# Kernel tuning notes

Measured on AMD Instinct MI355X. Metric: run time of the kernel, lower is better.

## Reference

```python
import jax, jax.numpy as jnp
import numpy as np

N_NODES = 101001  # n_user + n_item + n_attr + 1
EMBED = 64
N_EDGES = 2020020  # ~avg degree 20
EPS = 1e-12


def setup_inputs() -> dict:
    key = jax.random.key(0)
    ks = jax.random.split(key, 8)
    h0 = jax.random.normal(ks[0], (N_NODES, EMBED), dtype=jnp.float32)
    h_att = jax.random.normal(ks[1], (N_NODES, EMBED), dtype=jnp.float32)
    t_att = jax.random.normal(ks[2], (N_NODES, EMBED), dtype=jnp.float32)
    w1 = jax.random.normal(ks[3], (EMBED, EMBED), dtype=jnp.float32) * (1.0 / np.sqrt(EMBED))
    b1 = jnp.zeros((EMBED,), dtype=jnp.float32)
    w2 = jax.random.normal(ks[4], (EMBED, EMBED), dtype=jnp.float32) * (1.0 / np.sqrt(EMBED))
    b2 = jnp.zeros((EMBED,), dtype=jnp.float32)
    edge_row = jnp.sort(jax.random.randint(ks[5], (N_EDGES,), 0, N_NODES, dtype=jnp.int32))
    edge_col = jax.random.randint(ks[6], (N_EDGES,), 0, N_NODES, dtype=jnp.int32)
    return {"h0": h0, "h_att": h_att, "t_att": t_att, "w1": w1, "b1": b1,
            "w2": w2, "b2": b2, "edge_row": edge_row, "edge_col": edge_col}


def _edge_softmax(h_att, t_att, edge_row, edge_col, n):
    # per-source-node softmax over ragged neighbor lists (kg_pair)
    logits = jnp.sum(h_att[edge_row] * t_att[edge_col], axis=-1)  # [E]
    m = jax.ops.segment_max(logits, edge_row, num_segments=n)
    e = jnp.exp(logits - m[edge_row])
    s = jax.ops.segment_sum(e, edge_row, num_segments=n)
    return e / jnp.maximum(s[edge_row], EPS)  # [E]


def reference(h0, h_att, t_att, w1, b1, w2, b2, edge_row, edge_col):
    n, d = h0.shape
    w = _edge_softmax(h_att, t_att, edge_row, edge_col, n)  # sparse attention weights
    h = h0
    all_embedding = [h0]
    for (W, b) in ((w1, b1), (w2, b2)):  # k = 1, 2 of ProP_n_Layer
        # n_embedding = SpMM(sp_weight, h)
        msg = jax.ops.segment_sum(w[:, None] * h[edge_col], edge_row, num_segments=n)
        add = h + msg
        h = jax.nn.relu(add @ W.T + b)
        norm = h / jnp.maximum(jnp.linalg.norm(h, axis=-1, keepdims=True), EPS)
        all_embedding.append(norm)
        h = norm  # normalized embedding feeds the next propagation layer
    return jnp.stack(all_embedding, axis=0)  # [n_layer, N, D]
```

## Files before the change

### kernel.cpp

```cpp
#include <hip/hip_runtime.h>
#include <math.h>

#define EMBED 64

__device__ __forceinline__ float dot4(float4 a, float4 b) {
    return fmaf(a.x, b.x, fmaf(a.y, b.y, fmaf(a.z, b.z, a.w * b.w)));
}

__device__ __forceinline__ float red16(float d) {
    d += __shfl_xor(d, 1);
    d += __shfl_xor(d, 2);
    d += __shfl_xor(d, 4);
    d += __shfl_xor(d, 8);
    return d;
}

__global__ void copy_h0_kernel(const float* __restrict__ h0, float* __restrict__ out, int n4) {
    int i = blockIdx.x * blockDim.x + threadIdx.x;
    if (i < n4) ((float4*)out)[i] = ((const float4*)h0)[i];
}

__global__ void build_rowptr_kernel(const int* __restrict__ row, int* __restrict__ rp, int E, int N) {
    int i = blockIdx.x * blockDim.x + threadIdx.x;
    if (i >= E) return;
    if (i == 0) {
        int r0 = row[0];
        for (int r = 0; r <= r0; ++r) rp[r] = 0;
    } else {
        int a = row[i - 1], b = row[i];
        for (int r = a + 1; r <= b; ++r) rp[r] = i;
    }
    if (i == E - 1) {
        int rl = row[E - 1];
        for (int r = rl + 1; r <= N; ++r) rp[r] = E;
    }
}

__global__ void __launch_bounds__(256, 8) edge_logits_kernel(
        const float* __restrict__ ha, const float* __restrict__ ta,
        const int* __restrict__ row, const int* __restrict__ col,
        float* __restrict__ logits, int E, int totalWaves) {
    int wid = (blockIdx.x * blockDim.x + threadIdx.x) >> 6;
    int lane = threadIdx.x & 63;
    int eg = lane >> 4, q = lane & 15;
    const float4* ha4 = (const float4*)ha;
    const float4* ta4 = (const float4*)ta;

    for (int base = wid * 16; base < E; base += totalWaves * 16) {
        int j0 = base + eg, j1 = base + 4 + eg, j2 = base + 8 + eg, j3 = base + 12 + eg;
        int i0 = min(j0, E - 1), i1 = min(j1, E - 1);
        int i2 = min(j2, E - 1), i3 = min(j3, E - 1);
        int r0 = row[i0], r1 = row[i1], r2 = row[i2], r3 = row[i3];
        int c0 = col[i0], c1 = col[i1], c2 = col[i2], c3 = col[i3];
        float4 t0 = ta4[(size_t)c0 * 16 + q];
        float4 t1 = ta4[(size_t)c1 * 16 + q];
        float4 t2 = ta4[(size_t)c2 * 16 + q];
        float4 t3 = ta4[(size_t)c3 * 16 + q];
        float4 a0 = ha4[(size_t)r0 * 16 + q];
        float4 a1 = ha4[(size_t)r1 * 16 + q];
        float4 a2 = ha4[(size_t)r2 * 16 + q];
        float4 a3 = ha4[(size_t)r3 * 16 + q];
        float d0 = red16(dot4(a0, t0));
        float d1 = red16(dot4(a1, t1));
        float d2 = red16(dot4(a2, t2));
        float d3 = red16(dot4(a3, t3));
        if (q == 0) {
            if (j0 < E) logits[j0] = d0;
            if (j1 < E) logits[j1] = d1;
            if (j2 < E) logits[j2] = d2;
            if (j3 < E) logits[j3] = d3;
        }
    }
}

__global__ void __launch_bounds__(256) node_softmax_kernel(
        const int* __restrict__ rp, float* __restrict__ lw, int N) {
    int n = (blockIdx.x * blockDim.x + threadIdx.x) >> 6;
    int lane = threadIdx.x & 63;
    if (n >= N) return;
    int s = rp[n], t = rp[n + 1];
    int deg = t - s;
    if (deg <= 0) return;

    if (deg <= 64) {
        float v = (lane < deg) ? lw[s + lane] : -1e30f;
        float m = v;
        #pragma unroll
        for (int off = 32; off > 0; off >>= 1) m = fmaxf(m, __shfl_xor(m, off));
        float e = (lane < deg) ? __expf(v - m) : 0.f;
        float sum = e;
        #pragma unroll
        for (int off = 32; off > 0; off >>= 1) sum += __shfl_xor(sum, off);
        float inv = 1.f / fmaxf(sum, 1e-12f);
        if (lane < deg) lw[s + lane] = e * inv;
    } else {
        float m = -1e30f;
        for (int e = s + lane; e < t; e += 64) m = fmaxf(m, lw[e]);
        #pragma unroll
        for (int off = 32; off > 0; off >>= 1) m = fmaxf(m, __shfl_xor(m, off));
        float sum = 0.f;
        for (int e = s + lane; e < t; e += 64) sum += __expf(lw[e] - m);
        #pragma unroll
        for (int off = 32; off > 0; off >>= 1) sum += __shfl_xor(sum, off);
        float inv = 1.f / fmaxf(sum, 1e-12f);
        for (int e = s + lane; e < t; e += 64) lw[e] = __expf(lw[e] - m) * inv;
    }
}

__global__ void __launch_bounds__(256, 8) spmm_kernel(
        const float* __restrict__ h_in, const int* __restrict__ col,
        const float* __restrict__ ew, const int* __restrict__ rp,
        float* __restrict__ add_out, int N, int totalWaves) {
    int wid = (blockIdx.x * blockDim.x + threadIdx.x) >> 6;
    int lane = threadIdx.x & 63;
    int eg = lane >> 4, q = lane & 15;
    const float4* h4 = (const float4*)h_in;

    for (int n = wid; n < N; n += totalWaves) {
        int s = rp[n], t = rp[n + 1];
        float4 self = h4[(size_t)n * 16 + q];
        float4 a0 = make_float4(0.f, 0.f, 0.f, 0.f);
        float4 a1 = make_float4(0.f, 0.f, 0.f, 0.f);
        int e0 = s;
        for (; e0 + 16 <= t; e0 += 16) {
            int i0 = e0 + eg, i1 = e0 + 4 + eg, i2 = e0 + 8 + eg, i3 = e0 + 12 + eg;
            int c0 = col[i0], c1 = col[i1], c2 = col[i2], c3 = col[i3];
            float w0 = ew[i0], w1 = ew[i1], w2 = ew[i2], w3 = ew[i3];
            float4 v0 = h4[(size_t)c0 * 16 + q];
            float4 v1 = h4[(size_t)c1 * 16 + q];
            float4 v2 = h4[(size_t)c2 * 16 + q];
            float4 v3 = h4[(size_t)c3 * 16 + q];
            a0.x = fmaf(w0, v0.x, a0.x); a0.y = fmaf(w0, v0.y, a0.y);
            a0.z = fmaf(w0, v0.z, a0.z); a0.w = fmaf(w0, v0.w, a0.w);
            a1.x = fmaf(w1, v1.x, a1.x); a1.y = fmaf(w1, v1.y, a1.y);
            a1.z = fmaf(w1, v1.z, a1.z); a1.w = fmaf(w1, v1.w, a1.w);
            a0.x = fmaf(w2, v2.x, a0.x); a0.y = fmaf(w2, v2.y, a0.y);
            a0.z = fmaf(w2, v2.z, a0.z); a0.w = fmaf(w2, v2.w, a0.w);
            a1.x = fmaf(w3, v3.x, a1.x); a1.y = fmaf(w3, v3.y, a1.y);
            a1.z = fmaf(w3, v3.z, a1.z); a1.w = fmaf(w3, v3.w, a1.w);
        }
        if (e0 < t) {
            int j0 = e0 + eg, j1 = e0 + 4 + eg, j2 = e0 + 8 + eg, j3 = e0 + 12 + eg;
            int i0 = min(j0, t - 1), i1 = min(j1, t - 1);
            int i2 = min(j2, t - 1), i3 = min(j3, t - 1);
            int c0 = col[i0], c1 = col[i1], c2 = col[i2], c3 = col[i3];
            float w0 = (j0 < t) ? ew[i0] : 0.f;
            float w1 = (j1 < t) ? ew[i1] : 0.f;
            float w2 = (j2 < t) ? ew[i2] : 0.f;
            float w3 = (j3 < t) ? ew[i3] : 0.f;
            float4 v0 = h4[(size_t)c0 * 16 + q];
            float4 v1 = h4[(size_t)c1 * 16 + q];
            float4 v2 = h4[(size_t)c2 * 16 + q];
            float4 v3 = h4[(size_t)c3 * 16 + q];
            a0.x = fmaf(w0, v0.x, a0.x); a0.y = fmaf(w0, v0.y, a0.y);
            a0.z = fmaf(w0, v0.z, a0.z); a0.w = fmaf(w0, v0.w, a0.w);
            a1.x = fmaf(w1, v1.x, a1.x); a1.y = fmaf(w1, v1.y, a1.y);
            a1.z = fmaf(w1, v1.z, a1.z); a1.w = fmaf(w1, v1.w, a1.w);
            a0.x = fmaf(w2, v2.x, a0.x); a0.y = fmaf(w2, v2.y, a0.y);
            a0.z = fmaf(w2, v2.z, a0.z); a0.w = fmaf(w2, v2.w, a0.w);
            a1.x = fmaf(w3, v3.x, a1.x); a1.y = fmaf(w3, v3.y, a1.y);
            a1.z = fmaf(w3, v3.z, a1.z); a1.w = fmaf(w3, v3.w, a1.w);
        }
        a0.x += a1.x; a0.y += a1.y; a0.z += a1.z; a0.w += a1.w;
        a0.x += __shfl_xor(a0.x, 16); a0.y += __shfl_xor(a0.y, 16);
        a0.z += __shfl_xor(a0.z, 16); a0.w += __shfl_xor(a0.w, 16);
        a0.x += __shfl_xor(a0.x, 32); a0.y += __shfl_xor(a0.y, 32);
        a0.z += __shfl_xor(a0.z, 32); a0.w += __shfl_xor(a0.w, 32);
        if (eg == 0) {
            float4 r;
            r.x = self.x + a0.x; r.y = self.y + a0.y;
            r.z = self.z + a0.z; r.w = self.w + a0.w;
            ((float4*)add_out)[(size_t)n * 16 + q] = r;
        }
    }
}

__global__ void __launch_bounds__(256, 4) dense_kernel(
        const float* __restrict__ W, const float* __restrict__ b,
        float* __restrict__ io, int N, int totalWaves) {
    __shared__ float4 rbuf[4][17];
    int wid = (blockIdx.x * blockDim.x + threadIdx.x) >> 6;
    int lane = threadIdx.x & 63;
    int ws = threadIdx.x >> 6;

    float4 Wr[16];
    const float4* W4 = (const float4*)W;
    #pragma unroll
    for (int p = 0; p < 16; ++p) Wr[p] = W4[lane * 16 + p];
    float bias = b[lane];
    float* rb = (float*)&rbuf[ws][0];

    float vcur = 0.f;
    if (wid < N) vcur = io[(size_t)wid * EMBED + lane];

    for (int n = wid; n < N; n += totalWaves) {
        rb[lane] = vcur;
        int n2 = n + totalWaves;
        float vnext = 0.f;
        if (n2 < N) vnext = io[(size_t)n2 * EMBED + lane];

        float x0 = bias, x1 = 0.f, x2 = 0.f, x3 = 0.f;
        #pragma unroll
        for (int j = 0; j < 4; ++j) {
            float4 a0 = rbuf[ws][4 * j + 0];
            float4 a1 = rbuf[ws][4 * j + 1];
            float4 a2 = rbuf[ws][4 * j + 2];
            float4 a3 = rbuf[ws][4 * j + 3];
            float4 w0 = Wr[4 * j + 0], w1 = Wr[4 * j + 1];
            float4 w2 = Wr[4 * j + 2], w3 = Wr[4 * j + 3];
            x0 = fmaf(a0.x, w0.x, x0); x0 = fmaf(a0.y, w0.y, x0);
            x0 = fmaf(a0.z, w0.z, x0); x0 = fmaf(a0.w, w0.w, x0);
            x1 = fmaf(a1.x, w1.x, x1); x1 = fmaf(a1.y, w1.y, x1);
            x1 = fmaf(a1.z, w1.z, x1); x1 = fmaf(a1.w, w1.w, x1);
            x2 = fmaf(a2.x, w2.x, x2); x2 = fmaf(a2.y, w2.y, x2);
            x2 = fmaf(a2.z, w2.z, x2); x2 = fmaf(a2.w, w2.w, x2);
            x3 = fmaf(a3.x, w3.x, x3); x3 = fmaf(a3.y, w3.y, x3);
            x3 = fmaf(a3.z, w3.z, x3); x3 = fmaf(a3.w, w3.w, x3);
        }
        float x = fmaxf((x0 + x1) + (x2 + x3), 0.f);

        float ss = x * x;
        #pragma unroll
        for (int off = 32; off > 0; off >>= 1) ss += __shfl_xor(ss, off);
        float scale = 1.f / fmaxf(sqrtf(ss), 1e-12f);
        io[(size_t)n * EMBED + lane] = x * scale;
        vcur = vnext;
    }
}

extern "C" void kernel_launch(void* const* d_in, const int* in_sizes, int n_in,
                              void* d_out, int out_size, void* d_ws, size_t ws_size,
                              hipStream_t stream) {
    const float* h0   = (const float*)d_in[0];
    const float* ha   = (const float*)d_in[1];
    const float* ta   = (const float*)d_in[2];
    const float* w1   = (const float*)d_in[3];
    const float* b1   = (const float*)d_in[4];
    const float* w2   = (const float*)d_in[5];
    const float* b2   = (const float*)d_in[6];
    const int*   erow = (const int*)d_in[7];
    const int*   ecol = (const int*)d_in[8];

    const int N = in_sizes[0] / EMBED;
    const int E = in_sizes[7];
    float* out = (float*)d_out;

    int*   rp = (int*)d_ws;
    size_t rp_bytes = ((size_t)(N + 1) * sizeof(int) + 255) & ~(size_t)255;
    float* ew = (float*)((char*)d_ws + rp_bytes);

    {
        int n4 = N * EMBED / 4;
        copy_h0_kernel<<<(n4 + 255) / 256, 256, 0, stream>>>(h0, out, n4);
    }
    build_rowptr_kernel<<<(E + 255) / 256, 256, 0, stream>>>(erow, rp, E, N);
    edge_logits_kernel<<<2048, 256, 0, stream>>>(ha, ta, erow, ecol, ew, E, 2048 * 4);
    {
        int waves_per_block = 256 / 64;
        int blocks = (N + waves_per_block - 1) / waves_per_block;
        node_softmax_kernel<<<blocks, 256, 0, stream>>>(rp, ew, N);
    }

    float* out1 = out + (size_t)N * EMBED;
    float* out2 = out + 2 * (size_t)N * EMBED;
    spmm_kernel<<<2048, 256, 0, stream>>>(h0, ecol, ew, rp, out1, N, 2048 * 4);
    dense_kernel<<<1024, 256, 0, stream>>>(w1, b1, out1, N, 1024 * 4);
    spmm_kernel<<<2048, 256, 0, stream>>>(out1, ecol, ew, rp, out2, N, 2048 * 4);
    dense_kernel<<<1024, 256, 0, stream>>>(w2, b2, out2, N, 1024 * 4);
}
```

Baseline: 462.1 us.

## Fuse SpMM with dense layer and merge setup kernels to cut launches

Merges the rowptr build into the edge-logits kernel and the h0 copy into the softmax kernel. Fuses each SpMM with its following dense+ReLU+L2-normalize step, passing the aggregated row to the matmul through per-wave LDS instead of a global round trip. This removes four kernel launches and one write plus re-read of the intermediate per layer. In exchange the fused kernel holds the 64-float weight rows in registers, which may lower occupancy for the gather-heavy SpMM part, and it relies on an explicit lgkmcnt wait rather than a barrier for the intra-wave LDS handoff.

Result: faster. 416.7 us, median of 2 (-9.8%).

```diff
diff --git a/kernel.cpp b/kernel.cpp
--- a/kernel.cpp
+++ b/kernel.cpp
@@ -15,32 +15,28 @@
     return d;
 }
 
-__global__ void copy_h0_kernel(const float* __restrict__ h0, float* __restrict__ out, int n4) {
-    int i = blockIdx.x * blockDim.x + threadIdx.x;
-    if (i < n4) ((float4*)out)[i] = ((const float4*)h0)[i];
-}
-
-__global__ void build_rowptr_kernel(const int* __restrict__ row, int* __restrict__ rp, int E, int N) {
-    int i = blockIdx.x * blockDim.x + threadIdx.x;
-    if (i >= E) return;
-    if (i == 0) {
-        int r0 = row[0];
-        for (int r = 0; r <= r0; ++r) rp[r] = 0;
-    } else {
-        int a = row[i - 1], b = row[i];
-        for (int r = a + 1; r <= b; ++r) rp[r] = i;
-    }
-    if (i == E - 1) {
-        int rl = row[E - 1];
-        for (int r = rl + 1; r <= N; ++r) rp[r] = E;
-    }
-}
-
-__global__ void __launch_bounds__(256, 8) edge_logits_kernel(
+__global__ void __launch_bounds__(256, 8) rowptr_logits_kernel(
         const float* __restrict__ ha, const float* __restrict__ ta,
         const int* __restrict__ row, const int* __restrict__ col,
-        float* __restrict__ logits, int E, int totalWaves) {
-    int wid = (blockIdx.x * blockDim.x + threadIdx.x) >> 6;
+        int* __restrict__ rp, float* __restrict__ logits,
+        int E, int N, int totalThreads, int totalWaves) {
+    int tid = blockIdx.x * blockDim.x + threadIdx.x;
+
+    for (int i = tid; i < E; i += totalThreads) {
+        if (i == 0) {
+            int r0 = row[0];
+            for (int r = 0; r <= r0; ++r) rp[r] = 0;
+        } else {
+            int a = row[i - 1], b = row[i];
+            for (int r = a + 1; r <= b; ++r) rp[r] = i;
+        }
+        if (i == E - 1) {
+            int rl = row[E - 1];
+            for (int r = rl + 1; r <= N; ++r) rp[r] = E;
+        }
+    }
+
+    int wid = tid >> 6;
     int lane = threadIdx.x & 63;
     int eg = lane >> 4, q = lane & 15;
     const float4* ha4 = (const float4*)ha;
@@ -73,48 +69,64 @@
     }
 }
 
-__global__ void __launch_bounds__(256) node_softmax_kernel(
-        const int* __restrict__ rp, float* __restrict__ lw, int N) {
-    int n = (blockIdx.x * blockDim.x + threadIdx.x) >> 6;
+__global__ void __launch_bounds__(256) copy_softmax_kernel(
+        const float* __restrict__ h0, float* __restrict__ out0, int n4,
+        const int* __restrict__ rp, float* __restrict__ lw, int N,
+        int totalThreads, int totalWaves) {
+    int tid = blockIdx.x * blockDim.x + threadIdx.x;
+    for (int i = tid; i < n4; i += totalThreads)
+        ((float4*)out0)[i] = ((const float4*)h0)[i];
+
+    int wid = tid >> 6;
     int lane = threadIdx.x & 63;
-    if (n >= N) return;
-    int s = rp[n], t = rp[n + 1];
-    int deg = t - s;
-    if (deg <= 0) return;
-
-    if (deg <= 64) {
-        float v = (lane < deg) ? lw[s + lane] : -1e30f;
-        float m = v;
-        #pragma unroll
-        for (int off = 32; off > 0; off >>= 1) m = fmaxf(m, __shfl_xor(m, off));
-        float e = (lane < deg) ? __expf(v - m) : 0.f;
-        float sum = e;
-        #pragma unroll
-        for (int off = 32; off > 0; off >>= 1) sum += __shfl_xor(sum, off);
-        float inv = 1.f / fmaxf(sum, 1e-12f);
-        if (lane < deg) lw[s + lane] = e * inv;
-    } else {
-        float m = -1e30f;
-        for (int e = s + lane; e < t; e += 64) m = fmaxf(m, lw[e]);
-        #pragma unroll
-        for (int off = 32; off > 0; off >>= 1) m = fmaxf(m, __shfl_xor(m, off));
-        float sum = 0.f;
-        for (int e = s + lane; e < t; e += 64) sum += __expf(lw[e] - m);
-        #pragma unroll
-        for (int off = 32; off > 0; off >>= 1) sum += __shfl_xor(sum, off);
-        float inv = 1.f / fmaxf(sum, 1e-12f);
-        for (int e = s + lane; e < t; e += 64) lw[e] = __expf(lw[e] - m) * inv;
-    }
-}
-
-__global__ void __launch_bounds__(256, 8) spmm_kernel(
-        const float* __restrict__ h_in, const int* __restrict__ col,
-        const float* __restrict__ ew, const int* __restrict__ rp,
-        float* __restrict__ add_out, int N, int totalWaves) {
+    for (int n = wid; n < N; n += totalWaves) {
+        int s = rp[n], t = rp[n + 1];
+        int deg = t - s;
+        if (deg <= 0) continue;
+        if (deg <= 64) {
+            float v = (lane < deg) ? lw[s + lane] : -1e30f;
+            float m = v;
+            #pragma unroll
+            for (int off = 32; off > 0; off >>= 1) m = fmaxf(m, __shfl_xor(m, off));
+            float e = (lane < deg) ? __expf(v - m) : 0.f;
+            float sum = e;
+            #pragma unroll
+            for (int off = 32; off > 0; off >>= 1) sum += __shfl_xor(sum, off);
+            float inv = 1.f / fmaxf(sum, 1e-12f);
+            if (lane < deg) lw[s + lane] = e * inv;
+        } else {
+            float m = -1e30f;
+            for (int e = s + lane; e < t; e += 64) m = fmaxf(m, lw[e]);
+            #pragma unroll
+            for (int off = 32; off > 0; off >>= 1) m = fmaxf(m, __shfl_xor(m, off));
+            float sum = 0.f;
+            for (int e = s + lane; e < t; e += 64) sum += __expf(lw[e] - m);
+            #pragma unroll
+            for (int off = 32; off > 0; off >>= 1) sum += __shfl_xor(sum, off);
+            float inv = 1.f / fmaxf(sum, 1e-12f);
+            for (int e = s + lane; e < t; e += 64) lw[e] = __expf(lw[e] - m) * inv;
+        }
+    }
+}
+
+__global__ void __launch_bounds__(256, 4) prop_layer_kernel(
+        const float* __restrict__ h_in,
+        const float* __restrict__ W, const float* __restrict__ b,
+        const int* __restrict__ col, const float* __restrict__ ew,
+        const int* __restrict__ rp,
+        float* __restrict__ out, int N, int totalWaves) {
+    __shared__ float4 rbuf[4][17];
     int wid = (blockIdx.x * blockDim.x + threadIdx.x) >> 6;
     int lane = threadIdx.x & 63;
+    int ws = threadIdx.x >> 6;
     int eg = lane >> 4, q = lane & 15;
     const float4* h4 = (const float4*)h_in;
+
+    float4 Wr[16];
+    const float4* W4 = (const float4*)W;
+    #pragma unroll
+    for (int p = 0; p < 16; ++p) Wr[p] = W4[lane * 16 + p];
+    float bias = b[lane];
 
     for (int n = wid; n < N; n += totalWaves) {
         int s = rp[n], t = rp[n + 1];
@@ -166,56 +178,32 @@
         a0.z += __shfl_xor(a0.z, 16); a0.w += __shfl_xor(a0.w, 16);
         a0.x += __shfl_xor(a0.x, 32); a0.y += __shfl_xor(a0.y, 32);
         a0.z += __shfl_xor(a0.z, 32); a0.w += __shfl_xor(a0.w, 32);
+
         if (eg == 0) {
             float4 r;
             r.x = self.x + a0.x; r.y = self.y + a0.y;
             r.z = self.z + a0.z; r.w = self.w + a0.w;
-            ((float4*)add_out)[(size_t)n * 16 + q] = r;
-        }
-    }
-}
-
-__global__ void __launch_bounds__(256, 4) dense_kernel(
-        const float* __restrict__ W, const float* __restrict__ b,
-        float* __restrict__ io, int N, int totalWaves) {
-    __shared__ float4 rbuf[4][17];
-    int wid = (blockIdx.x * blockDim.x + threadIdx.x) >> 6;
-    int lane = threadIdx.x & 63;
-    int ws = threadIdx.x >> 6;
-
-    float4 Wr[16];
-    const float4* W4 = (const float4*)W;
-    #pragma unroll
-    for (int p = 0; p < 16; ++p) Wr[p] = W4[lane * 16 + p];
-    float bias = b[lane];
-    float* rb = (float*)&rbuf[ws][0];
-
-    float vcur = 0.f;
-    if (wid < N) vcur = io[(size_t)wid * EMBED + lane];
-
-    for (int n = wid; n < N; n += totalWaves) {
-        rb[lane] = vcur;
-        int n2 = n + totalWaves;
-        float vnext = 0.f;
-        if (n2 < N) vnext = io[(size_t)n2 * EMBED + lane];
+            rbuf[ws][q] = r;
+        }
+        asm volatile("s_waitcnt lgkmcnt(0)" ::: "memory");
 
         float x0 = bias, x1 = 0.f, x2 = 0.f, x3 = 0.f;
         #pragma unroll
         for (int j = 0; j < 4; ++j) {
-            float4 a0 = rbuf[ws][4 * j + 0];
-            float4 a1 = rbuf[ws][4 * j + 1];
-            float4 a2 = rbuf[ws][4 * j + 2];
-            float4 a3 = rbuf[ws][4 * j + 3];
+            float4 b0 = rbuf[ws][4 * j + 0];
+            float4 b1 = rbuf[ws][4 * j + 1];
+            float4 b2 = rbuf[ws][4 * j + 2];
+            float4 b3 = rbuf[ws][4 * j + 3];
             float4 w0 = Wr[4 * j + 0], w1 = Wr[4 * j + 1];
             float4 w2 = Wr[4 * j + 2], w3 = Wr[4 * j + 3];
-            x0 = fmaf(a0.x, w0.x, x0); x0 = fmaf(a0.y, w0.y, x0);
-            x0 = fmaf(a0.z, w0.z, x0); x0 = fmaf(a0.w, w0.w, x0);
-            x1 = fmaf(a1.x, w1.x, x1); x1 = fmaf(a1.y, w1.y, x1);
-            x1 = fmaf(a1.z, w1.z, x1); x1 = fmaf(a1.w, w1.w, x1);
-            x2 = fmaf(a2.x, w2.x, x2); x2 = fmaf(a2.y, w2.y, x2);
-            x2 = fmaf(a2.z, w2.z, x2); x2 = fmaf(a2.w, w2.w, x2);
-            x3 = fmaf(a3.x, w3.x, x3); x3 = fmaf(a3.y, w3.y, x3);
-            x3 = fmaf(a3.z, w3.z, x3); x3 = fmaf(a3.w, w3.w, x3);
+            x0 = fmaf(b0.x, w0.x, x0); x0 = fmaf(b0.y, w0.y, x0);
+            x0 = fmaf(b0.z, w0.z, x0); x0 = fmaf(b0.w, w0.w, x0);
+            x1 = fmaf(b1.x, w1.x, x1); x1 = fmaf(b1.y, w1.y, x1);
+            x1 = fmaf(b1.z, w1.z, x1); x1 = fmaf(b1.w, w1.w, x1);
+            x2 = fmaf(b2.x, w2.x, x2); x2 = fmaf(b2.y, w2.y, x2);
+            x2 = fmaf(b2.z, w2.z, x2); x2 = fmaf(b2.w, w2.w, x2);
+            x3 = fmaf(b3.x, w3.x, x3); x3 = fmaf(b3.y, w3.y, x3);
+            x3 = fmaf(b3.z, w3.z, x3); x3 = fmaf(b3.w, w3.w, x3);
         }
         float x = fmaxf((x0 + x1) + (x2 + x3), 0.f);
 
@@ -223,8 +211,7 @@
         #pragma unroll
         for (int off = 32; off > 0; off >>= 1) ss += __shfl_xor(ss, off);
         float scale = 1.f / fmaxf(sqrtf(ss), 1e-12f);
-        io[(size_t)n * EMBED + lane] = x * scale;
-        vcur = vnext;
+        out[(size_t)n * EMBED + lane] = x * scale;
     }
 }
 
@@ -249,22 +236,14 @@
     size_t rp_bytes = ((size_t)(N + 1) * sizeof(int) + 255) & ~(size_t)255;
     float* ew = (float*)((char*)d_ws + rp_bytes);
 
-    {
-        int n4 = N * EMBED / 4;
-        copy_h0_kernel<<<(n4 + 255) / 256, 256, 0, stream>>>(h0, out, n4);
-    }
-    build_rowptr_kernel<<<(E + 255) / 256, 256, 0, stream>>>(erow, rp, E, N);
-    edge_logits_kernel<<<2048, 256, 0, stream>>>(ha, ta, erow, ecol, ew, E, 2048 * 4);
-    {
-        int waves_per_block = 256 / 64;
-        int blocks = (N + waves_per_block - 1) / waves_per_block;
-        node_softmax_kernel<<<blocks, 256, 0, stream>>>(rp, ew, N);
-    }
+    rowptr_logits_kernel<<<2048, 256, 0, stream>>>(
+        ha, ta, erow, ecol, rp, ew, E, N, 2048 * 256, 2048 * 4);
+
+    copy_softmax_kernel<<<2048, 256, 0, stream>>>(
+        h0, out, N * EMBED / 4, rp, ew, N, 2048 * 256, 2048 * 4);
 
     float* out1 = out + (size_t)N * EMBED;
     float* out2 = out + 2 * (size_t)N * EMBED;
-    spmm_kernel<<<2048, 256, 0, stream>>>(h0, ecol, ew, rp, out1, N, 2048 * 4);
-    dense_kernel<<<1024, 256, 0, stream>>>(w1, b1, out1, N, 1024 * 4);
-    spmm_kernel<<<2048, 256, 0, stream>>>(out1, ecol, ew, rp, out2, N, 2048 * 4);
-    dense_kernel<<<1024, 256, 0, stream>>>(w2, b2, out2, N, 1024 * 4);
-}
+    prop_layer_kernel<<<1024, 256, 0, stream>>>(h0,   w1, b1, ecol, ew, rp, out1, N, 1024 * 4);
+    prop_layer_kernel<<<1024, 256, 0, stream>>>(out1, w2, b2, ecol, ew, rp, out2, N, 1024 * 4);
+}
```
